# Optimization experiments

Hardware: AMD Instinct MI355X
Metric: run time of the kernel (lower is better)

Reference implementation:

```python
import jax, jax.numpy as jnp
import numpy as np

N, T, H, L, E, F, CN, CG = 20000, 2, 128, 4, 320000, 514, 3, 2
EPS = 1e-7  # GENConv message epsilon


def _ln(x, g, b):
    mu = jnp.mean(x, axis=-1, keepdims=True)
    var = jnp.mean((x - mu) ** 2, axis=-1, keepdims=True)
    return (x - mu) / jnp.sqrt(var + 1e-5) * g + b


def _genconv(x, src, dst, e, W1, b1, g1, be1, W2, b2, t, n):
    # message: relu(x_j + edge_attr) + eps
    msg = jax.nn.relu(x[src] + e) + EPS  # [E,H]
    # softmax aggregation with learnable temperature t, grouped by dst
    logits = msg * t
    m = jax.ops.segment_max(logits, dst, num_segments=n)
    m = jnp.where(jnp.isfinite(m), m, 0.0)  # guard empty segments
    ex = jnp.exp(logits - m[dst])
    denom = jax.ops.segment_sum(ex, dst, num_segments=n)
    alpha = ex / (denom[dst] + 1e-16)
    agg = jax.ops.segment_sum(msg * alpha, dst, num_segments=n)  # [N,H]
    out = agg + x  # residual with root node (x_r)
    # MLP: Lin(H,2H) -> LayerNorm -> ReLU -> Lin(2H,H)
    h1 = jax.nn.relu(_ln(out @ W1 + b1, g1, be1))
    return h1 @ W2 + b2


def _attn(x, Wq, Wk, Wv, gamma):
    # x: [N, T, H]; channel (transform-axis) self-attention, gamma-gated residual
    q = jnp.einsum('tc,nch->nth', Wq, x)
    k = jnp.einsum('tc,nch->nth', Wk, x)
    v = jnp.einsum('tc,nch->nth', Wv, x)
    a = jax.nn.softmax(jnp.einsum('nth,nsh->nts', q, k), axis=-1)
    o = jnp.einsum('nts,nsh->nth', a, v)
    return gamma * o + x


def setup_inputs() -> dict:
    key = jax.random.key(0)
    ks = iter(jax.random.split(key, 48))

    def nrm(sh, s=0.02):
        return jax.random.normal(next(ks), sh, dtype=jnp.float32) * s

    inp = {}
    inp['node_feature'] = jax.random.normal(next(ks), (N, F), dtype=jnp.float32)
    inp['edge_index'] = jax.random.randint(next(ks), (T, 2, E), 0, N, dtype=jnp.int32)
    inp['edge_attr'] = jax.random.normal(next(ks), (T, E, 2), dtype=jnp.float32)
    # encoders
    inp['Wne'] = nrm((F, H)); inp['bne'] = jnp.zeros((H,), jnp.float32)
    inp['Wee'] = nrm((2, H)); inp['bee'] = jnp.zeros((H,), jnp.float32)
    # per-layer GENConv MLP params (stacked over L)
    inp['W1'] = nrm((L, H, 2 * H)); inp['b1'] = jnp.zeros((L, 2 * H), jnp.float32)
    inp['g1'] = jnp.ones((L, 2 * H), jnp.float32); inp['be1'] = jnp.zeros((L, 2 * H), jnp.float32)
    inp['W2'] = nrm((L, 2 * H, H)); inp['b2'] = jnp.zeros((L, H), jnp.float32)
    # DeepGCNLayer LayerNorms
    inp['dg'] = jnp.ones((L, H), jnp.float32); inp['db'] = jnp.zeros((L, H), jnp.float32)
    # learnable temperatures
    inp['t'] = jnp.ones((L,), jnp.float32)
    # node attention + head
    inp['Wq_n'] = nrm((T, T), 0.2); inp['Wk_n'] = nrm((T, T), 0.2); inp['Wv_n'] = nrm((T, T), 0.2)
    inp['gamma_n'] = jnp.float32(0.5)
    inp['Wn1'] = nrm((T * H, T * H)); inp['bn1'] = jnp.zeros((T * H,), jnp.float32)
    inp['Wn2'] = nrm((T * H, CN)); inp['bn2'] = jnp.zeros((CN,), jnp.float32)
    # graph attention + head
    inp['Wq_g'] = nrm((T, T), 0.2); inp['Wk_g'] = nrm((T, T), 0.2); inp['Wv_g'] = nrm((T, T), 0.2)
    inp['gamma_g'] = jnp.float32(0.5)
    inp['Wg1'] = nrm((T * H, T * H)); inp['bg1'] = jnp.zeros((T * H,), jnp.float32)
    inp['Wg2'] = nrm((T * H, CG)); inp['bg2'] = jnp.zeros((CG,), jnp.float32)
    return inp


def reference(node_feature, edge_index, edge_attr, Wne, bne, Wee, bee,
              W1, b1, g1, be1, W2, b2, dg, db, t,
              Wq_n, Wk_n, Wv_n, gamma_n, Wn1, bn1, Wn2, bn2,
              Wq_g, Wk_g, Wv_g, gamma_g, Wg1, bg1, Wg2, bg2):
    embs = []
    for ti in range(T):
        x = node_feature @ Wne + bne           # node_encoder
        e = edge_attr[ti] @ Wee + bee          # edge_encoder
        src, dst = edge_index[ti, 0], edge_index[ti, 1]
        # layers[0].conv applied directly
        x = _genconv(x, src, dst, e, W1[0], b1[0], g1[0], be1[0], W2[0], b2[0], t[0], N)
        # res+ DeepGCN blocks
        for l in range(1, L):
            h = jax.nn.relu(_ln(x, dg[l], db[l]))  # dropout p=0.1 is identity in eval
            x = x + _genconv(h, src, dst, e, W1[l], b1[l], g1[l], be1[l], W2[l], b2[l], t[l], N)
        x = jax.nn.relu(_ln(x, dg[0], db[0]))
        embs.append(x)
    emb = jnp.stack(embs, axis=1)  # [N, T, H]

    a = _attn(emb, Wq_n, Wk_n, Wv_n, gamma_n).reshape(N, T * H)
    node = jax.nn.relu(a @ Wn1 + bn1) @ Wn2 + bn2
    node = jax.nn.log_softmax(node, axis=-1)

    g = _attn(emb, Wq_g, Wk_g, Wv_g, gamma_g).reshape(N, T * H)
    gp = jnp.mean(g, axis=0, keepdims=True)  # global_mean_pool (single graph)
    gp = jax.nn.relu(gp @ Wg1 + bg1) @ Wg2 + bg2
    gp = jax.nn.log_softmax(gp, axis=-1)
    return (node, gp)
```

## Files before the change

### kernel.cpp

```cpp
#include <hip/hip_runtime.h>

#define NN 20000
#define TT 2
#define HH 128
#define LL 4
#define EE 320000
#define FF 514
#define CN 3
#define CG 2
#define MP 20096

typedef __bf16 bf16x8 __attribute__((ext_vector_type(8)));
typedef __bf16 bf16x4 __attribute__((ext_vector_type(4)));
typedef __bf16 bf16x2 __attribute__((ext_vector_type(2)));
typedef float f32x4 __attribute__((ext_vector_type(4)));

struct __align__(8) Edge { int src; __bf16 ea0, ea1; };

__device__ inline float wave_sum(float v) {
#pragma unroll
  for (int off = 32; off; off >>= 1) v += __shfl_xor(v, off);
  return v;
}
__device__ inline float red16(float v) {
  v += __shfl_xor(v, 1); v += __shfl_xor(v, 2);
  v += __shfl_xor(v, 4); v += __shfl_xor(v, 8);
  return v;
}

__device__ __forceinline__ float fexp2(float x) {
#if __has_builtin(__builtin_amdgcn_exp2f)
  return __builtin_amdgcn_exp2f(x);
#else
  return exp2f(x);
#endif
}

__device__ __forceinline__ void gload_lds16(const void* g, void* l) {
  __builtin_amdgcn_global_load_lds(
      (const __attribute__((address_space(1))) unsigned int*)g,
      (__attribute__((address_space(3))) unsigned int*)l, 16, 0, 0);
}

#define ENCB (MP / 64)
#define SCB 2500
#define CHUNK 5000
__global__ __launch_bounds__(256) void enc_scatter_kernel(
    const __bf16* __restrict__ A, const __bf16* __restrict__ BT,
    const float* __restrict__ bias, __bf16* __restrict__ C,
    const int* __restrict__ edge_index, const float* __restrict__ edge_attr,
    int* __restrict__ cursor, Edge* __restrict__ edges) {
  __shared__ __bf16 As[2][64][32];
  __shared__ __bf16 Bs[2][128][32];
  const int tid = threadIdx.x;
  if (blockIdx.x >= ENCB) {
    int chunk = blockIdx.x & 7;
    int i = ((blockIdx.x - ENCB) >> 3) * 256 + tid;
    if (i >= 2 * EE) return;
    int ti = (i >= EE) ? 1 : 0;
    int e = i - ti * EE;
    const int* srcp = edge_index + (size_t)ti * 2 * EE;
    int d = srcp[EE + e];
    int gnode = ti * NN + d;
    if (gnode / CHUNK != chunk) return;
    int s = srcp[e];
    float2 ea = ((const float2*)edge_attr)[(size_t)ti * EE + e];
    int pos = atomicAdd(&cursor[gnode], 1);
    Edge ed;
    ed.src = s + ti * MP;
    ed.ea0 = (__bf16)ea.x; ed.ea1 = (__bf16)ea.y;
    __builtin_memcpy(&edges[pos], &ed, sizeof(Edge));
    return;
  }
  const int K = 576;
  const int lane = tid & 63, w = tid >> 6;
  const int bm = blockIdx.x * 64;
  const int wr = (w >> 1) * 32, wc = (w & 1) * 64;
  const int fr = lane & 15, fq = lane >> 4;
  const int rowA = tid >> 2, chA = (tid & 3) * 8;
  const __bf16* Ab = A + (size_t)(bm + rowA) * K + chA;
  const __bf16* Bb = BT + (size_t)rowA * K + chA;
  const __bf16* Bb2 = Bb + (size_t)64 * K;
  f32x4 acc[2][4] = {};
#define STAGE(buf, k0)                                  \
  do {                                                  \
    gload_lds16(Ab + (k0), &As[buf][rowA][chA]);        \
    gload_lds16(Bb + (k0), &Bs[buf][rowA][chA]);        \
    gload_lds16(Bb2 + (k0), &Bs[buf][rowA + 64][chA]);  \
  } while (0)
  STAGE(0, 0);
  __syncthreads();
  int cur = 0;
  for (int k0 = 0; k0 < K; k0 += 32) {
    if (k0 + 32 < K) STAGE(cur ^ 1, k0 + 32);
    bf16x8 af[2], bq[4];
#pragma unroll
    for (int m = 0; m < 2; ++m)
      af[m] = *(const bf16x8*)&As[cur][wr + m * 16 + fr][fq * 8];
#pragma unroll
    for (int n = 0; n < 4; ++n)
      bq[n] = *(const bf16x8*)&Bs[cur][wc + n * 16 + fr][fq * 8];
#pragma unroll
    for (int m = 0; m < 2; ++m)
#pragma unroll
      for (int n = 0; n < 4; ++n)
        acc[m][n] =
            __builtin_amdgcn_mfma_f32_16x16x32_bf16(af[m], bq[n], acc[m][n], 0, 0, 0);
    __syncthreads();
    cur ^= 1;
  }
#undef STAGE
#pragma unroll
  for (int m = 0; m < 2; ++m) {
#pragma unroll
    for (int n = 0; n < 4; ++n) {
#pragma unroll
      for (int j = 0; j < 4; ++j) {
        int gm = bm + wr + m * 16 + fq * 4 + j;
        int gn = wc + n * 16 + fr;
        if (gm < NN) {
          __bf16 c = (__bf16)(acc[m][n][j] + bias[gn]);
          C[(size_t)gm * 128 + gn] = c;
          C[(size_t)(gm + MP) * 128 + gn] = c;
        }
      }
    }
  }
}

template <int EPI>
__global__ __launch_bounds__(256) void gemm256(
    const __bf16* __restrict__ A, const __bf16* __restrict__ BT,
    const float* __restrict__ bias, const float* __restrict__ g,
    const float* __restrict__ be, const float* __restrict__ W2h,
    const float* __restrict__ b2h, void* __restrict__ outp, int M, int K) {
  __shared__ __bf16 As[2][64][32];
  __shared__ __bf16 Bs[2][256][32];
  const int tid = threadIdx.x;
  const int lane = tid & 63, w = tid >> 6;
  const int bm = blockIdx.x * 64;
  const int wr = w * 16;
  const int fr = lane & 15, fq = lane >> 4;
  const int rowA = tid >> 2, chA = (tid & 3) * 8;
  const __bf16* Ab = A + (size_t)(bm + rowA) * K + chA;
  const __bf16* Bb = BT + (size_t)rowA * K + chA;
  f32x4 acc[16] = {};

#define STG(buf, k0)                                                \
  do {                                                              \
    gload_lds16(Ab + (k0), &As[buf][rowA][chA]);                    \
    _Pragma("unroll") for (int r = 0; r < 4; ++r)                   \
        gload_lds16(Bb + (size_t)(r * 64) * K + (k0),               \
                    &Bs[buf][rowA + r * 64][chA]);                  \
  } while (0)

  STG(0, 0);
  __syncthreads();
  int cur = 0;
  for (int k0 = 0; k0 < K; k0 += 32) {
    if (k0 + 32 < K) STG(cur ^ 1, k0 + 32);
    bf16x8 af = *(const bf16x8*)&As[cur][wr + fr][fq * 8];
#pragma unroll
    for (int n = 0; n < 16; ++n) {
      bf16x8 bq = *(const bf16x8*)&Bs[cur][n * 16 + fr][fq * 8];
      acc[n] = __builtin_amdgcn_mfma_f32_16x16x32_bf16(af, bq, acc[n], 0, 0, 0);
    }
    __syncthreads();
    cur ^= 1;
  }
#undef STG

  float cb[16];
#pragma unroll
  for (int n = 0; n < 16; ++n) cb[n] = bias[n * 16 + fr];

  if constexpr (EPI == 0) {
    float gv[16], bev[16];
#pragma unroll
    for (int n = 0; n < 16; ++n) {
      gv[n] = g[n * 16 + fr];
      bev[n] = be[n * 16 + fr];
    }
    __bf16* outb = (__bf16*)outp;
#pragma unroll
    for (int j = 0; j < 4; ++j) {
      float cj[16], s = 0.f, s2 = 0.f;
#pragma unroll
      for (int n = 0; n < 16; ++n) {
        float c = acc[n][j] + cb[n];
        cj[n] = c; s += c; s2 += c * c;
      }
      s = red16(s); s2 = red16(s2);
      float mu = s * (1.f / 256);
      float var = fmaxf(s2 * (1.f / 256) - mu * mu, 0.f);
      float rr = rsqrtf(var + 1e-5f);
      int gm = bm + wr + fq * 4 + j;
      __bf16* op = outb + (size_t)gm * 256;
#pragma unroll
      for (int n = 0; n < 16; ++n) {
        float y = (cj[n] - mu) * rr * gv[n] + bev[n];
        op[n * 16 + fr] = (__bf16)fmaxf(y, 0.f);
      }
    }
  } else {
    float w0[16], w1[16], w2[16];
#pragma unroll
    for (int n = 0; n < 16; ++n) {
      int col = n * 16 + fr;
      w0[n] = W2h[col * 3 + 0];
      w1[n] = W2h[col * 3 + 1];
      w2[n] = W2h[col * 3 + 2];
    }
    float* outf = (float*)outp;
#pragma unroll
    for (int j = 0; j < 4; ++j) {
      float p0 = 0.f, p1 = 0.f, p2 = 0.f;
#pragma unroll
      for (int n = 0; n < 16; ++n) {
        float h = fmaxf(acc[n][j] + cb[n], 0.f);
        p0 += h * w0[n]; p1 += h * w1[n]; p2 += h * w2[n];
      }
      p0 = red16(p0); p1 = red16(p1); p2 = red16(p2);
      int gm = bm + wr + fq * 4 + j;
      if (fr == 0 && gm < M) {
        float l0 = p0 + b2h[0], l1 = p1 + b2h[1], l2 = p2 + b2h[2];
        float m = fmaxf(l0, fmaxf(l1, l2));
        float lse = m + logf(__expf(l0 - m) + __expf(l1 - m) + __expf(l2 - m));
        outf[(size_t)gm * 3 + 0] = l0 - lse;
        outf[(size_t)gm * 3 + 1] = l1 - lse;
        outf[(size_t)gm * 3 + 2] = l2 - lse;
      }
    }
  }
}

template <int MODE>
__global__ __launch_bounds__(256) void gemm_lin2(
    const __bf16* __restrict__ A, const __bf16* __restrict__ BT,
    const float* __restrict__ bias, float* __restrict__ xres,
    const float* __restrict__ g, const float* __restrict__ be,
    void* __restrict__ lnout) {
  __shared__ __bf16 As[2][64][32];
  __shared__ __bf16 Bs[2][128][32];
  __shared__ float redS[64][2], redS2[64][2];
  const int tid = threadIdx.x;
  const int lane = tid & 63, w = tid >> 6;
  const int bm = blockIdx.x * 64;
  const int wr = (w >> 1) * 32, wc = (w & 1) * 64;
  const int fr = lane & 15, fq = lane >> 4;
  const int rowA = tid >> 2, chA = (tid & 3) * 8;
  const __bf16* Ab = A + (size_t)(bm + rowA) * 256 + chA;
  const __bf16* Bb = BT + (size_t)rowA * 256 + chA;
  const __bf16* Bb2 = Bb + (size_t)64 * 256;
  f32x4 acc[2][4] = {};

#define STAGE(buf, k0)                                  \
  do {                                                  \
    gload_lds16(Ab + (k0), &As[buf][rowA][chA]);        \
    gload_lds16(Bb + (k0), &Bs[buf][rowA][chA]);        \
    gload_lds16(Bb2 + (k0), &Bs[buf][rowA + 64][chA]);  \
  } while (0)

  STAGE(0, 0);
  __syncthreads();
  int cur = 0;
  for (int k0 = 0; k0 < 256; k0 += 32) {
    if (k0 + 32 < 256) STAGE(cur ^ 1, k0 + 32);
    bf16x8 af[2], bq[4];
#pragma unroll
    for (int m = 0; m < 2; ++m)
      af[m] = *(const bf16x8*)&As[cur][wr + m * 16 + fr][fq * 8];
#pragma unroll
    for (int n = 0; n < 4; ++n)
      bq[n] = *(const bf16x8*)&Bs[cur][wc + n * 16 + fr][fq * 8];
#pragma unroll
    for (int m = 0; m < 2; ++m)
#pragma unroll
      for (int n = 0; n < 4; ++n)
        acc[m][n] =
            __builtin_amdgcn_mfma_f32_16x16x32_bf16(af[m], bq[n], acc[m][n], 0, 0, 0);
    __syncthreads();
    cur ^= 1;
  }
#undef STAGE

  float cv[2][4][4];
#pragma unroll
  for (int m = 0; m < 2; ++m) {
    int r0 = wr + m * 16 + fq * 4;
#pragma unroll
    for (int j = 0; j < 4; ++j) {
      int gm = bm + r0 + j;
      float s = 0.f, s2 = 0.f;
#pragma unroll
      for (int n = 0; n < 4; ++n) {
        float c = acc[m][n][j] + bias[wc + n * 16 + fr];
        if (MODE != 0) c += xres[(size_t)gm * 128 + wc + n * 16 + fr];
        cv[m][n][j] = c;
        s += c; s2 += c * c;
      }
      s = red16(s); s2 = red16(s2);
      if (fr == 0) {
        redS[r0 + j][w & 1] = s;
        redS2[r0 + j][w & 1] = s2;
      }
    }
  }
  __syncthreads();
#pragma unroll
  for (int m = 0; m < 2; ++m) {
    int r0 = wr + m * 16 + fq * 4;
#pragma unroll
    for (int j = 0; j < 4; ++j) {
      int r = r0 + j;
      int gm = bm + r;
      float S = redS[r][0] + redS[r][1];
      float S2 = redS2[r][0] + redS2[r][1];
      float mu = S * (1.f / 128);
      float var = fmaxf(S2 * (1.f / 128) - mu * mu, 0.f);
      float rr = rsqrtf(var + 1e-5f);
      if constexpr (MODE < 2) {
        float* xp = xres + (size_t)gm * 128;
        __bf16* hp = (__bf16*)lnout + (size_t)gm * 128;
#pragma unroll
        for (int n = 0; n < 4; ++n) {
          int col = wc + n * 16 + fr;
          float c = cv[m][n][j];
          xp[col] = c;
          float y = (c - mu) * rr * g[col] + be[col];
          hp[col] = (__bf16)fmaxf(y, 0.f);
        }
      } else {
        int half = gm >= MP;
        int node = gm - half * MP;
        if (node < NN) {
          float* ep = (float*)lnout + (size_t)node * 256 + half * 128;
#pragma unroll
          for (int n = 0; n < 4; ++n) {
            int col = wc + n * 16 + fr;
            float y = (cv[m][n][j] - mu) * rr * g[col] + be[col];
            ep[col] = fmaxf(y, 0.f);
          }
        }
      }
    }
  }
}

struct WtDesc { const float* src; __bf16* dst; int K, N, Kpad; };
struct WtDescs { WtDesc d[10]; };
#define NF2B 20079
#define PADB 2422
#define WTB 2880
#define CNTB 2500

__global__ void prep_kernel(const float* __restrict__ nf_src,
                            __bf16* __restrict__ nf_dst, WtDescs descs,
                            const int* __restrict__ edge_index,
                            int* __restrict__ deg, float* __restrict__ gp_sum) {
  int b = blockIdx.x, tid = threadIdx.x;
  if (b < NF2B) {
    int i = b * 256 + tid;
    if (i >= NN * FF / 2) return;
    int row = i / 257;
    int col = (i - row * 257) * 2;
    float2 v = ((const float2*)nf_src)[i];
    bf16x2 o; o[0] = (__bf16)v.x; o[1] = (__bf16)v.y;
    *(bf16x2*)(nf_dst + (size_t)row * 576 + col) = o;
  } else if (b < NF2B + PADB) {
    int i = (b - NF2B) * 256 + tid;
    if (i >= NN * 31) return;
    int row = i / 31, j = i - row * 31;
    bf16x2 z; z[0] = (__bf16)0.f; z[1] = (__bf16)0.f;
    *(bf16x2*)(nf_dst + (size_t)row * 576 + 514 + 2 * j) = z;
  } else if (b < NF2B + PADB + WTB) {
    int wb = b - NF2B - PADB;
    WtDesc de = descs.d[wb / 288];
    int idx = (wb % 288) * 256 + tid;
    if (idx >= de.N * de.Kpad) return;
    int n = idx / de.Kpad, k = idx - n * de.Kpad;
    float v = (k < de.K) ? de.src[(size_t)k * de.N + n] : 0.f;
    de.dst[idx] = (__bf16)v;
  } else if (b < NF2B + PADB + WTB + CNTB) {
    int i = (b - NF2B - PADB - WTB) * 256 + tid;
    if (i >= 2 * EE) return;
    int ti = (i >= EE) ? 1 : 0;
    int e = i - ti * EE;
    int d = edge_index[(size_t)ti * 2 * EE + EE + e];
    atomicAdd(&deg[ti * NN + d], 1);
  } else {
    gp_sum[tid] = 0.f;
  }
}

__global__ __launch_bounds__(1024) void scan2_kernel(
    const int* __restrict__ deg_all, int* __restrict__ rowptr,
    int* __restrict__ cursor) {
  const int ti = blockIdx.x;
  const int* deg = deg_all + ti * NN;
  __shared__ int sums[1024];
  int tid = threadIdx.x;
  int chunk = (NN + 1023) / 1024;
  int begin = tid * chunk, end = min(begin + chunk, NN);
  int s = 0;
  for (int i = begin; i < end; ++i) s += deg[i];
  sums[tid] = s;
  __syncthreads();
  for (int off = 1; off < 1024; off <<= 1) {
    int v = (tid >= off) ? sums[tid - off] : 0;
    __syncthreads();
    sums[tid] += v;
    __syncthreads();
  }
  int running = ti * EE + sums[tid] - s;
  for (int i = begin; i < end; ++i) {
    rowptr[ti * NN + i] = running;
    cursor[ti * NN + i] = running;
    running += deg[i];
  }
  if (tid == 0 && ti == 1) rowptr[2 * NN] = 2 * EE;
}

__global__ __launch_bounds__(256) void agg_kernel(
    const __bf16* __restrict__ xin, const int* __restrict__ rowptr,
    const Edge* __restrict__ edges, const float* __restrict__ Wee,
    const float* __restrict__ bee, const float* __restrict__ tptr, int layer,
    __bf16* __restrict__ out) {
  int wave = threadIdx.x >> 6, lane = threadIdx.x & 63;
  int b = blockIdx.x;
  int x8 = b & 7;
  int q = x8 >> 1;
  int par = x8 & 1;
  int ti = q >> 1, chh = q & 1;
  int group = (b >> 3) * 2 + par;
  int qq = lane >> 4, c15 = lane & 15;
  int node = group * 16 + wave * 4 + qq;
  int gnode = ti * NN + node;
  int xrow = ti * MP + node;
  float t2 = tptr[layer] * 1.4426950408889634f;
  int c0 = chh * 64 + c15 * 4;
  float den[4] = {}, num[4] = {};
  int e = rowptr[gnode];
  const int e1 = rowptr[gnode + 1];

  if (t2 > 0.f) {
    float w0p[4], w1p[4], bvp[4];
#pragma unroll
    for (int i = 0; i < 4; ++i) {
      w0p[i] = Wee[c0 + i] * t2;
      w1p[i] = Wee[HH + c0 + i] * t2;
      bvp[i] = bee[c0 + i] * t2;
    }
#define MLPF(XV, ED)                                                      \
  do {                                                                    \
    float eax = (float)(ED).ea0, eay = (float)(ED).ea1;                   \
    _Pragma("unroll") for (int i = 0; i < 4; ++i) {                       \
      float te = fmaf(eax, w0p[i], fmaf(eay, w1p[i], bvp[i]));            \
      float sm = fmaxf(fmaf((float)(XV)[i], t2, te), 0.f);                \
      float ex = fexp2(sm);                                               \
      den[i] += ex; num[i] = fmaf(sm, ex, num[i]);                        \
    }                                                                     \
  } while (0)
    for (; e + 2 <= e1; e += 2) {
      Edge E0 = edges[e];
      Edge E1 = edges[e + 1];
      bf16x4 x0 = *(const bf16x4*)(xin + (size_t)E0.src * HH + c0);
      bf16x4 x1 = *(const bf16x4*)(xin + (size_t)E1.src * HH + c0);
      MLPF(x0, E0);
      MLPF(x1, E1);
    }
    if (e < e1) {
      Edge E0 = edges[e];
      bf16x4 x0 = *(const bf16x4*)(xin + (size_t)E0.src * HH + c0);
      MLPF(x0, E0);
    }
#undef MLPF
    bf16x4 xr = *(const bf16x4*)(xin + (size_t)xrow * HH + c0);
    bf16x4 o;
#pragma unroll
    for (int i = 0; i < 4; ++i)
      o[i] = (__bf16)(num[i] / (t2 * (den[i] + 1e-16f)) + (float)xr[i]);
    *(bf16x4*)(out + (size_t)xrow * HH + c0) = o;
  } else {
    float w0[4], w1[4], bv[4];
#pragma unroll
    for (int i = 0; i < 4; ++i) {
      w0[i] = Wee[c0 + i];
      w1[i] = Wee[HH + c0 + i];
      bv[i] = bee[c0 + i];
    }
    for (; e < e1; ++e) {
      Edge E0 = edges[e];
      bf16x4 xv = *(const bf16x4*)(xin + (size_t)E0.src * HH + c0);
      float eax = (float)E0.ea0, eay = (float)E0.ea1;
#pragma unroll
      for (int i = 0; i < 4; ++i) {
        float m =
            fmaxf((float)xv[i] + eax * w0[i] + eay * w1[i] + bv[i], 0.f) + 1e-7f;
        float ex = fexp2(m * t2);
        den[i] += ex; num[i] += m * ex;
      }
    }
    bf16x4 xr = *(const bf16x4*)(xin + (size_t)xrow * HH + c0);
    bf16x4 o;
#pragma unroll
    for (int i = 0; i < 4; ++i)
      o[i] = (__bf16)(num[i] / (den[i] + 1e-16f) + (float)xr[i]);
    *(bf16x4*)(out + (size_t)xrow * HH + c0) = o;
  }
}

__global__ __launch_bounds__(256) void attn2_kernel(
    const float* __restrict__ emb, const float* __restrict__ Wq_n,
    const float* __restrict__ Wk_n, const float* __restrict__ Wv_n,
    const float* __restrict__ gn, const float* __restrict__ Wq_g,
    const float* __restrict__ Wk_g, const float* __restrict__ Wv_g,
    const float* __restrict__ gg, __bf16* __restrict__ outn,
    float* __restrict__ partial) {
  __shared__ float gsum[4][256];
  int wave = threadIdx.x >> 6, lane = threadIdx.x & 63;
  int tid = threadIdx.x;
  int n = blockIdx.x * 4 + wave;
  int c0 = lane * 2;
  const float* base = emb + (size_t)n * (2 * HH);
  float2 x0 = *(const float2*)(base + c0);
  float2 x1 = *(const float2*)(base + HH + c0);

#define ATTN_BODY(Wq, Wk, Wv, GAM, O0A, O0B, O1A, O1B)                        \
  {                                                                           \
    float gamma = *(GAM);                                                     \
    float wq00 = Wq[0], wq01 = Wq[1], wq10 = Wq[2], wq11 = Wq[3];             \
    float wk00 = Wk[0], wk01 = Wk[1], wk10 = Wk[2], wk11 = Wk[3];             \
    float wv00 = Wv[0], wv01 = Wv[1], wv10 = Wv[2], wv11 = Wv[3];             \
    float q0a = wq00 * x0.x + wq01 * x1.x, q0b = wq00 * x0.y + wq01 * x1.y;   \
    float q1a = wq10 * x0.x + wq11 * x1.x, q1b = wq10 * x0.y + wq11 * x1.y;   \
    float k0a = wk00 * x0.x + wk01 * x1.x, k0b = wk00 * x0.y + wk01 * x1.y;   \
    float k1a = wk10 * x0.x + wk11 * x1.x, k1b = wk10 * x0.y + wk11 * x1.y;   \
    float v0a = wv00 * x0.x + wv01 * x1.x, v0b = wv00 * x0.y + wv01 * x1.y;   \
    float v1a = wv10 * x0.x + wv11 * x1.x, v1b = wv10 * x0.y + wv11 * x1.y;   \
    float s00 = wave_sum(q0a * k0a + q0b * k0b);                              \
    float s01 = wave_sum(q0a * k1a + q0b * k1b);                              \
    float s10 = wave_sum(q1a * k0a + q1b * k0b);                              \
    float s11 = wave_sum(q1a * k1a + q1b * k1b);                              \
    float m0 = fmaxf(s00, s01);                                               \
    float e00 = __expf(s00 - m0), e01 = __expf(s01 - m0);                     \
    float i0 = 1.f / (e00 + e01);                                             \
    float a00 = e00 * i0, a01 = e01 * i0;                                     \
    float m1 = fmaxf(s10, s11);                                               \
    float e10 = __expf(s10 - m1), e11 = __expf(s11 - m1);                     \
    float i1 = 1.f / (e10 + e11);                                             \
    float a10 = e10 * i1, a11 = e11 * i1;                                     \
    O0A = gamma * (a00 * v0a + a01 * v1a) + x0.x;                             \
    O0B = gamma * (a00 * v0b + a01 * v1b) + x0.y;                             \
    O1A = gamma * (a10 * v0a + a11 * v1a) + x1.x;                             \
    O1B = gamma * (a10 * v0b + a11 * v1b) + x1.y;                             \
  }

  float n0a, n0b, n1a, n1b;
  ATTN_BODY(Wq_n, Wk_n, Wv_n, gn, n0a, n0b, n1a, n1b);
  __bf16* opn = outn + (size_t)n * (2 * HH);
  bf16x2 t0; t0[0] = (__bf16)n0a; t0[1] = (__bf16)n0b;
  bf16x2 t1; t1[0] = (__bf16)n1a; t1[1] = (__bf16)n1b;
  *(bf16x2*)(opn + c0) = t0;
  *(bf16x2*)(opn + HH + c0) = t1;

  float g0a, g0b, g1a, g1b;
  ATTN_BODY(Wq_g, Wk_g, Wv_g, gg, g0a, g0b, g1a, g1b);
  gsum[wave][c0] = g0a;
  gsum[wave][c0 + 1] = g0b;
  gsum[wave][128 + c0] = g1a;
  gsum[wave][129 + c0] = g1b;
  __syncthreads();
  partial[(size_t)blockIdx.x * 256 + tid] =
      gsum[0][tid] + gsum[1][tid] + gsum[2][tid] + gsum[3][tid];
#undef ATTN_BODY
}

__global__ __launch_bounds__(256) void pool_kernel(const float* __restrict__ partial,
                                                   float* __restrict__ gp_sum,
                                                   int nRows) {
  int c = threadIdx.x;
  float s = 0.f;
  for (int r = blockIdx.x; r < nRows; r += gridDim.x)
    s += partial[(size_t)r * 256 + c];
  atomicAdd(&gp_sum[c], s);
}

__global__ __launch_bounds__(256) void graph_head_kernel(
    const float* __restrict__ gp_sum, const float* __restrict__ Wg1,
    const float* __restrict__ bg1, const float* __restrict__ Wg2,
    const float* __restrict__ bg2, float* __restrict__ outp, float invN) {
  __shared__ float gp[256];
  __shared__ float h1[256];
  __shared__ float lg[2];
  int tid = threadIdx.x;
  gp[tid] = gp_sum[tid] * invN;
  __syncthreads();
  float acc = bg1[tid];
  for (int k = 0; k < 256; ++k) acc += gp[k] * Wg1[k * 256 + tid];
  h1[tid] = fmaxf(acc, 0.f);
  __syncthreads();
  if (tid < 2) {
    float l = bg2[tid];
    for (int c = 0; c < 256; ++c) l += h1[c] * Wg2[c * 2 + tid];
    lg[tid] = l;
  }
  __syncthreads();
  if (tid == 0) {
    float m = fmaxf(lg[0], lg[1]);
    float lse = m + logf(__expf(lg[0] - m) + __expf(lg[1] - m));
    outp[0] = lg[0] - lse;
    outp[1] = lg[1] - lse;
  }
}

extern "C" void kernel_launch(void* const* d_in, const int* in_sizes, int n_in,
                              void* d_out, int out_size, void* d_ws, size_t ws_size,
                              hipStream_t stream) {
  (void)in_sizes; (void)n_in; (void)out_size; (void)ws_size;
  const float* node_feature = (const float*)d_in[0];
  const int* edge_index = (const int*)d_in[1];
  const float* edge_attr = (const float*)d_in[2];
  const float* Wne = (const float*)d_in[3];
  const float* bne = (const float*)d_in[4];
  const float* Wee = (const float*)d_in[5];
  const float* bee = (const float*)d_in[6];
  const float* W1 = (const float*)d_in[7];
  const float* b1 = (const float*)d_in[8];
  const float* g1 = (const float*)d_in[9];
  const float* be1 = (const float*)d_in[10];
  const float* W2 = (const float*)d_in[11];
  const float* b2 = (const float*)d_in[12];
  const float* dg = (const float*)d_in[13];
  const float* db = (const float*)d_in[14];
  const float* tpar = (const float*)d_in[15];
  const float* Wq_n = (const float*)d_in[16];
  const float* Wk_n = (const float*)d_in[17];
  const float* Wv_n = (const float*)d_in[18];
  const float* gamma_n = (const float*)d_in[19];
  const float* Wn1 = (const float*)d_in[20];
  const float* bn1 = (const float*)d_in[21];
  const float* Wn2 = (const float*)d_in[22];
  const float* bn2 = (const float*)d_in[23];
  const float* Wq_g = (const float*)d_in[24];
  const float* Wk_g = (const float*)d_in[25];
  const float* Wv_g = (const float*)d_in[26];
  const float* gamma_g = (const float*)d_in[27];
  const float* Wg1 = (const float*)d_in[28];
  const float* bg1 = (const float*)d_in[29];
  const float* Wg2 = (const float*)d_in[30];
  const float* bg2 = (const float*)d_in[31];
  float* out = (float*)d_out;

  char* pc = (char*)d_ws;
  auto alloc = [&](size_t bytes) {
    char* r = pc;
    pc += (bytes + 255) & ~(size_t)255;
    return r;
  };
  float* xbuf = (float*)alloc((size_t)2 * MP * HH * 4);
  __bf16* hbuf_b = (__bf16*)alloc((size_t)2 * MP * HH * 2);
  __bf16* t256_b = (__bf16*)alloc((size_t)2 * MP * 256 * 2);
  float* emb = (float*)alloc((size_t)NN * 2 * HH * 4);
  __bf16* aggout_b = (__bf16*)alloc((size_t)2 * MP * HH * 2);
  __bf16* nf_b = (__bf16*)emb;
  __bf16* attnb = t256_b;
  float* partial = xbuf;
  __bf16* wt_ne = (__bf16*)alloc((size_t)128 * 576 * 2);
  __bf16* wt1 = (__bf16*)alloc((size_t)4 * 256 * 128 * 2);
  __bf16* wt2 = (__bf16*)alloc((size_t)4 * 128 * 256 * 2);
  __bf16* wtn1 = (__bf16*)alloc((size_t)256 * 256 * 2);
  float* gp_sum = (float*)alloc(256 * 4);
  int* deg = (int*)alloc((size_t)2 * NN * 4);
  int* cursor = (int*)alloc((size_t)2 * NN * 4);
  int* rowptr = (int*)alloc((size_t)(2 * NN + 2) * 4);
  Edge* edges = (Edge*)alloc((size_t)2 * EE * 8);

  const int gRows2 = 2 * MP / 64;

  WtDescs wd;
  wd.d[0] = {Wne, wt_ne, FF, HH, 576};
  for (int l = 0; l < 4; ++l)
    wd.d[1 + l] = {W1 + (size_t)l * HH * 256, wt1 + (size_t)l * 256 * HH, HH, 256, HH};
  for (int l = 0; l < 4; ++l)
    wd.d[5 + l] = {W2 + (size_t)l * 256 * HH, wt2 + (size_t)l * HH * 256, 256, HH, 256};
  wd.d[9] = {Wn1, wtn1, 256, 256, 256};

  hipMemsetAsync(deg, 0, 2 * NN * sizeof(int), stream);
  prep_kernel<<<NF2B + PADB + WTB + CNTB + 1, 256, 0, stream>>>(
      node_feature, nf_b, wd, edge_index, deg, gp_sum);
  scan2_kernel<<<2, 1024, 0, stream>>>(deg, rowptr, cursor);
  enc_scatter_kernel<<<ENCB + 8 * SCB, 256, 0, stream>>>(
      nf_b, wt_ne, bne, hbuf_b, edge_index, edge_attr, cursor, edges);

  for (int l = 0; l < LL; ++l) {
    agg_kernel<<<625 * 8, 256, 0, stream>>>(hbuf_b, rowptr, edges, Wee, bee, tpar,
                                            l, aggout_b);
    gemm256<0><<<gRows2, 256, 0, stream>>>(aggout_b, wt1 + (size_t)l * 256 * HH,
                                           b1 + l * 2 * HH, g1 + l * 2 * HH,
                                           be1 + l * 2 * HH, nullptr, nullptr, t256_b,
                                           2 * MP, HH);
    const __bf16* w2l = wt2 + (size_t)l * HH * 256;
    const float* b2l = b2 + l * HH;
    if (l == 0)
      gemm_lin2<0><<<gRows2, 256, 0, stream>>>(t256_b, w2l, b2l, xbuf, dg + 1 * HH,
                                               db + 1 * HH, hbuf_b);
    else if (l < LL - 1)
      gemm_lin2<1><<<gRows2, 256, 0, stream>>>(t256_b, w2l, b2l, xbuf,
                                               dg + (l + 1) * HH, db + (l + 1) * HH,
                                               hbuf_b);
    else
      gemm_lin2<2><<<gRows2, 256, 0, stream>>>(t256_b, w2l, b2l, xbuf, dg, db, emb);
  }

  attn2_kernel<<<NN / 4, 256, 0, stream>>>(emb, Wq_n, Wk_n, Wv_n, gamma_n, Wq_g,
                                           Wk_g, Wv_g, gamma_g, attnb, partial);
  gemm256<1><<<MP / 64, 256, 0, stream>>>(attnb, wtn1, bn1, nullptr, nullptr, Wn2,
                                          bn2, out, NN, 256);
  pool_kernel<<<128, 256, 0, stream>>>(partial, gp_sum, NN / 4);
  graph_head_kernel<<<1, 256, 0, stream>>>(gp_sum, Wg1, bg1, Wg2, bg2,
                                           out + (size_t)NN * CN, 1.0f / NN);
}
```

Measured before the change: 443.6 us.

## Vectorize prep and edge-scatter kernels with 8-wide work items and grid-stride loop

The prep kernel becomes a fixed-size grid-stride loop in which each thread converts 8 node-feature columns (padding included), 8 weight elements, or 8 degree counts at a time, replacing the many-block scalar version. The edge-scatter path in the encoder kernel now handles 8 edges per thread with one vectorized load of the destination indices. The aim is to cut block launch overhead and per-element instruction count, and to use wider memory accesses. The trade-off is that the strided weight-transpose reads become serial within each thread, and fewer threads are left to hide atomic latency.

```diff
diff --git a/kernel.cpp b/kernel.cpp
--- a/kernel.cpp
+++ b/kernel.cpp
@@ -43,7 +43,7 @@
 }
 
 #define ENCB (MP / 64)
-#define SCB 2500
+#define SSB 313
 #define CHUNK 5000
 __global__ __launch_bounds__(256) void enc_scatter_kernel(
     const __bf16* __restrict__ A, const __bf16* __restrict__ BT,
@@ -54,22 +54,28 @@
   __shared__ __bf16 Bs[2][128][32];
   const int tid = threadIdx.x;
   if (blockIdx.x >= ENCB) {
-    int chunk = blockIdx.x & 7;
-    int i = ((blockIdx.x - ENCB) >> 3) * 256 + tid;
-    if (i >= 2 * EE) return;
-    int ti = (i >= EE) ? 1 : 0;
-    int e = i - ti * EE;
+    int sb = blockIdx.x - ENCB;
+    int chunk = sb & 7;
+    int slice = sb >> 3;
+    int i0 = slice * 2048 + tid * 8;
+    if (i0 >= 2 * EE) return;
+    int ti = (i0 >= EE) ? 1 : 0;
+    int e0 = i0 - ti * EE;
     const int* srcp = edge_index + (size_t)ti * 2 * EE;
-    int d = srcp[EE + e];
-    int gnode = ti * NN + d;
-    if (gnode / CHUNK != chunk) return;
-    int s = srcp[e];
-    float2 ea = ((const float2*)edge_attr)[(size_t)ti * EE + e];
-    int pos = atomicAdd(&cursor[gnode], 1);
-    Edge ed;
-    ed.src = s + ti * MP;
-    ed.ea0 = (__bf16)ea.x; ed.ea1 = (__bf16)ea.y;
-    __builtin_memcpy(&edges[pos], &ed, sizeof(Edge));
+    int dst8[8];
+    __builtin_memcpy(dst8, srcp + EE + e0, 32);
+#pragma unroll
+    for (int j = 0; j < 8; ++j) {
+      int gnode = ti * NN + dst8[j];
+      if (gnode / CHUNK != chunk) continue;
+      int s = srcp[e0 + j];
+      float2 ea = ((const float2*)edge_attr)[(size_t)ti * EE + e0 + j];
+      int pos = atomicAdd(&cursor[gnode], 1);
+      Edge ed;
+      ed.src = s + ti * MP;
+      ed.ea0 = (__bf16)ea.x; ed.ea1 = (__bf16)ea.y;
+      __builtin_memcpy(&edges[pos], &ed, sizeof(Edge));
+    }
     return;
   }
   const int K = 576;
@@ -347,49 +353,65 @@
   }
 }
 
-struct WtDesc { const float* src; __bf16* dst; int K, N, Kpad; };
+struct WtDesc { const float* src; __bf16* dst; int K, N, Kpad, gbase; };
 struct WtDescs { WtDesc d[10]; };
-#define NF2B 20079
-#define PADB 2422
-#define WTB 2880
-#define CNTB 2500
-
-__global__ void prep_kernel(const float* __restrict__ nf_src,
-                            __bf16* __restrict__ nf_dst, WtDescs descs,
-                            const int* __restrict__ edge_index,
-                            int* __restrict__ deg, float* __restrict__ gp_sum) {
-  int b = blockIdx.x, tid = threadIdx.x;
-  if (b < NF2B) {
-    int i = b * 256 + tid;
-    if (i >= NN * FF / 2) return;
-    int row = i / 257;
-    int col = (i - row * 257) * 2;
-    float2 v = ((const float2*)nf_src)[i];
-    bf16x2 o; o[0] = (__bf16)v.x; o[1] = (__bf16)v.y;
-    *(bf16x2*)(nf_dst + (size_t)row * 576 + col) = o;
-  } else if (b < NF2B + PADB) {
-    int i = (b - NF2B) * 256 + tid;
-    if (i >= NN * 31) return;
-    int row = i / 31, j = i - row * 31;
-    bf16x2 z; z[0] = (__bf16)0.f; z[1] = (__bf16)0.f;
-    *(bf16x2*)(nf_dst + (size_t)row * 576 + 514 + 2 * j) = z;
-  } else if (b < NF2B + PADB + WTB) {
-    int wb = b - NF2B - PADB;
-    WtDesc de = descs.d[wb / 288];
-    int idx = (wb % 288) * 256 + tid;
-    if (idx >= de.N * de.Kpad) return;
-    int n = idx / de.Kpad, k = idx - n * de.Kpad;
-    float v = (k < de.K) ? de.src[(size_t)k * de.N + n] : 0.f;
-    de.dst[idx] = (__bf16)v;
-  } else if (b < NF2B + PADB + WTB + CNTB) {
-    int i = (b - NF2B - PADB - WTB) * 256 + tid;
-    if (i >= 2 * EE) return;
-    int ti = (i >= EE) ? 1 : 0;
-    int e = i - ti * EE;
-    int d = edge_index[(size_t)ti * 2 * EE + EE + e];
-    atomicAdd(&deg[ti * NN + d], 1);
-  } else {
-    gp_sum[tid] = 0.f;
+#define NFG 1440000
+#define WTG 50176
+#define CTG 80000
+#define PREPG 2048
+
+__global__ __launch_bounds__(256) void prep_kernel(
+    const float* __restrict__ nf_src, __bf16* __restrict__ nf_dst, WtDescs descs,
+    const int* __restrict__ edge_index, int* __restrict__ deg,
+    float* __restrict__ gp_sum) {
+  const int tid = threadIdx.x;
+  if (blockIdx.x == 0) gp_sum[tid] = 0.f;
+  const int TOT = NFG + WTG + CTG;
+  for (int g = blockIdx.x * 256 + tid; g < TOT; g += PREPG * 256) {
+    if (g < NFG) {
+      int row = g / 72, colg = g - row * 72;
+      int col0 = colg * 8;
+      bf16x8 o;
+      if (col0 + 8 <= FF) {
+        float v[8];
+        __builtin_memcpy(v, nf_src + (size_t)row * FF + col0, 32);
+#pragma unroll
+        for (int i = 0; i < 8; ++i) o[i] = (__bf16)v[i];
+      } else {
+#pragma unroll
+        for (int i = 0; i < 8; ++i) {
+          int col = col0 + i;
+          o[i] = (__bf16)((col < FF) ? nf_src[(size_t)row * FF + col] : 0.f);
+        }
+      }
+      *(bf16x8*)(nf_dst + (size_t)row * 576 + col0) = o;
+    } else if (g < NFG + WTG) {
+      int wb = g - NFG;
+      int di = 0;
+#pragma unroll
+      for (int t = 1; t < 10; ++t)
+        if (wb >= descs.d[t].gbase) di = t;
+      WtDesc de = descs.d[di];
+      int local = wb - de.gbase;
+      int kg8 = de.Kpad >> 3;
+      int n = local / kg8, k0 = (local - n * kg8) * 8;
+      bf16x8 o;
+#pragma unroll
+      for (int i = 0; i < 8; ++i) {
+        int k = k0 + i;
+        o[i] = (__bf16)((k < de.K) ? de.src[(size_t)k * de.N + n] : 0.f);
+      }
+      *(bf16x8*)(de.dst + (size_t)n * de.Kpad + k0) = o;
+    } else {
+      int i0 = (g - NFG - WTG) * 8;
+      int ti = (i0 >= EE) ? 1 : 0;
+      int e0 = i0 - ti * EE;
+      int dst8[8];
+      __builtin_memcpy(dst8, edge_index + (size_t)ti * 2 * EE + EE + e0, 32);
+      int* dbase = deg + ti * NN;
+#pragma unroll
+      for (int j = 0; j < 8; ++j) atomicAdd(&dbase[dst8[j]], 1);
+    }
   }
 }
 
@@ -679,18 +701,25 @@
   const int gRows2 = 2 * MP / 64;
 
   WtDescs wd;
-  wd.d[0] = {Wne, wt_ne, FF, HH, 576};
-  for (int l = 0; l < 4; ++l)
-    wd.d[1 + l] = {W1 + (size_t)l * HH * 256, wt1 + (size_t)l * 256 * HH, HH, 256, HH};
-  for (int l = 0; l < 4; ++l)
-    wd.d[5 + l] = {W2 + (size_t)l * 256 * HH, wt2 + (size_t)l * HH * 256, 256, HH, 256};
-  wd.d[9] = {Wn1, wtn1, 256, 256, 256};
+  int gb = 0;
+  wd.d[0] = {Wne, wt_ne, FF, HH, 576, gb}; gb += HH * 576 / 8;
+  for (int l = 0; l < 4; ++l) {
+    wd.d[1 + l] = {W1 + (size_t)l * HH * 256, wt1 + (size_t)l * 256 * HH, HH, 256,
+                   HH, gb};
+    gb += 256 * HH / 8;
+  }
+  for (int l = 0; l < 4; ++l) {
+    wd.d[5 + l] = {W2 + (size_t)l * 256 * HH, wt2 + (size_t)l * HH * 256, 256, HH,
+                   256, gb};
+    gb += HH * 256 / 8;
+  }
+  wd.d[9] = {Wn1, wtn1, 256, 256, 256, gb};
 
   hipMemsetAsync(deg, 0, 2 * NN * sizeof(int), stream);
-  prep_kernel<<<NF2B + PADB + WTB + CNTB + 1, 256, 0, stream>>>(
-      node_feature, nf_b, wd, edge_index, deg, gp_sum);
+  prep_kernel<<<PREPG, 256, 0, stream>>>(node_feature, nf_b, wd, edge_index, deg,
+                                         gp_sum);
   scan2_kernel<<<2, 1024, 0, stream>>>(deg, rowptr, cursor);
-  enc_scatter_kernel<<<ENCB + 8 * SCB, 256, 0, stream>>>(
+  enc_scatter_kernel<<<ENCB + 8 * SSB, 256, 0, stream>>>(
       nf_b, wt_ne, bne, hbuf_b, edge_index, edge_attr, cursor, edges);
 
   for (int l = 0; l < LL; ++l) {
```

Result: no change. 442.5 us (-0.2%).
